# Kernel tuning notes

Measured on AMD Instinct MI355X. Metric: run time of the kernel, lower is better.

Reference implementation:

```python
import jax, jax.numpy as jnp
import numpy as np

IN_F = 1024
OUT_F = 512
BATCH = 256
NO_EDGE_OFFSET_T_NORM = 2.0    # identity element offset for min over [0,1] inputs
NO_EDGE_OFFSET_T_CONORM = -1.0 # identity element offset for max over [0,1] inputs


def setup_inputs() -> dict:
    key = jax.random.key(0)
    k1, k2 = jax.random.split(key)
    # fuzzy truth-value inputs in [0, 1]
    x = jax.random.uniform(k1, (BATCH, IN_F), dtype=jnp.float32)
    # logits for gumbel-softmax edge-type selection (module inits to ones)
    edge_type_count = jnp.ones((OUT_F, IN_F, 2), dtype=jnp.float32)
    # uniform noise used to build gumbel noise deterministically
    uniform_noise = jax.random.uniform(k2, (OUT_F, IN_F, 2), dtype=jnp.float32)
    return {"x": x, "edge_type_count": edge_type_count, "uniform_noise": uniform_noise}


def reference(x, edge_type_count, uniform_noise):
    eps = 1e-10
    # hard gumbel-softmax -> only the argmax index is consumed downstream
    gumbel = -jnp.log(-jnp.log(uniform_noise + eps) + eps)
    idx = jnp.argmax(edge_type_count + gumbel, axis=-1)   # [OUT_F, IN_F]; 0 = edge, 1 = no_edge
    is_no_edge = idx == 1                                  # [OUT_F, IN_F]

    # operators cycle [T_Norm.min, T_Conorm.max] across output nodes
    tnorm = (jnp.arange(OUT_F) % 2) == 0                   # [OUT_F]
    offset = jnp.where(tnorm, NO_EDGE_OFFSET_T_NORM, NO_EDGE_OFFSET_T_CONORM).astype(x.dtype)

    # edge value: x for a real edge, 0 + per-operator no_edge offset otherwise
    vals = jnp.where(is_no_edge[None, :, :], offset[None, :, None], x[:, None, :])  # [B, OUT_F, IN_F]

    # per-node t-norm (min) or t-conorm (max) reduction over in_features
    out = jnp.where(tnorm[None, :], jnp.min(vals, axis=-1), jnp.max(vals, axis=-1))  # [B, OUT_F]
    return out
```

## Files before the change

### kernel.cpp

```cpp
#include <hip/hip_runtime.h>
#include <stdint.h>

#define IN_F   1024
#define OUT_F  512
#define BATCH  256

__global__ __launch_bounds__(256) void mask_kernel(
    const float* __restrict__ etc,
    const float* __restrict__ un,
    unsigned long long* __restrict__ mask_t)
{
    int o = blockIdx.x >> 2;
    int c = blockIdx.x & 3;
    int j = threadIdx.x >> 6;
    int l = threadIdx.x & 63;
    int i = c * 256 + l * 4 + j;
    int p = o * IN_F + i;

    float2 e = ((const float2*)etc)[p];
    float2 u = ((const float2*)un)[p];

    float s0 = u.x + 1e-10f;
    float l0 = (float)log((double)s0);
    float m0 = -l0 + 1e-10f;
    float g0 = -(float)log((double)m0);
    float t0 = e.x + g0;

    float s1 = u.y + 1e-10f;
    float l1 = (float)log((double)s1);
    float m1 = -l1 + 1e-10f;
    float g1 = -(float)log((double)m1);
    float t1 = e.y + g1;

    unsigned long long bits = __ballot(!(t1 > t0));
    if (l == 0) mask_t[o * 16 + c * 4 + j] = bits;
}

__device__ __forceinline__ float csel(unsigned long long m, float xv, float sent) {
    float r;
    asm("v_cndmask_b32 %0, %1, %2, %3" : "=v"(r) : "v"(sent), "v"(xv), "s"(m));
    return r;
}

__global__ __launch_bounds__(256, 8) void reduce_kernel(
    const float* __restrict__ x,
    const unsigned long long* __restrict__ mask_t,
    float* __restrict__ out)
{
    int wave = threadIdx.x >> 6;
    int lane = threadIdx.x & 63;
    int W = blockIdx.x * 4 + wave;
    int b  = __builtin_amdgcn_readfirstlane(W >> 7);
    int r  = W & 127;
    int parity = __builtin_amdgcn_readfirstlane(r & 1);
    int oq = __builtin_amdgcn_readfirstlane(r >> 1);

    const float4* x4 = (const float4*)(x + b * IN_F);

    int o0 = ((oq * 4 + 0) << 1) | parity;
    int o1 = ((oq * 4 + 1) << 1) | parity;
    int o2 = ((oq * 4 + 2) << 1) | parity;
    int o3 = ((oq * 4 + 3) << 1) | parity;
    const unsigned long long* mw0 = mask_t + o0 * 16;
    const unsigned long long* mw1 = mask_t + o1 * 16;
    const unsigned long long* mw2 = mask_t + o2 * 16;
    const unsigned long long* mw3 = mask_t + o3 * 16;

    if (parity == 0) {
        float a0 = 2.0f, a1 = 2.0f, a2 = 2.0f, a3 = 2.0f;
        const float S = 2.0f;
        #pragma unroll
        for (int c = 0; c < 4; ++c) {
            float4 xv = x4[c * 64 + lane];
            a0 = fminf(a0, csel(mw0[c*4+0], xv.x, S));
            a0 = fminf(a0, csel(mw0[c*4+1], xv.y, S));
            a0 = fminf(a0, csel(mw0[c*4+2], xv.z, S));
            a0 = fminf(a0, csel(mw0[c*4+3], xv.w, S));
            a1 = fminf(a1, csel(mw1[c*4+0], xv.x, S));
            a1 = fminf(a1, csel(mw1[c*4+1], xv.y, S));
            a1 = fminf(a1, csel(mw1[c*4+2], xv.z, S));
            a1 = fminf(a1, csel(mw1[c*4+3], xv.w, S));
            a2 = fminf(a2, csel(mw2[c*4+0], xv.x, S));
            a2 = fminf(a2, csel(mw2[c*4+1], xv.y, S));
            a2 = fminf(a2, csel(mw2[c*4+2], xv.z, S));
            a2 = fminf(a2, csel(mw2[c*4+3], xv.w, S));
            a3 = fminf(a3, csel(mw3[c*4+0], xv.x, S));
            a3 = fminf(a3, csel(mw3[c*4+1], xv.y, S));
            a3 = fminf(a3, csel(mw3[c*4+2], xv.z, S));
            a3 = fminf(a3, csel(mw3[c*4+3], xv.w, S));
        }
        #pragma unroll
        for (int d = 32; d; d >>= 1) {
            a0 = fminf(a0, __shfl_xor(a0, d, 64));
            a1 = fminf(a1, __shfl_xor(a1, d, 64));
            a2 = fminf(a2, __shfl_xor(a2, d, 64));
            a3 = fminf(a3, __shfl_xor(a3, d, 64));
        }
        if (lane == 0) {
            float* ob = out + b * OUT_F;
            ob[o0] = a0; ob[o1] = a1; ob[o2] = a2; ob[o3] = a3;
        }
    } else {
        float a0 = -1.0f, a1 = -1.0f, a2 = -1.0f, a3 = -1.0f;
        const float S = -1.0f;
        #pragma unroll
        for (int c = 0; c < 4; ++c) {
            float4 xv = x4[c * 64 + lane];
            a0 = fmaxf(a0, csel(mw0[c*4+0], xv.x, S));
            a0 = fmaxf(a0, csel(mw0[c*4+1], xv.y, S));
            a0 = fmaxf(a0, csel(mw0[c*4+2], xv.z, S));
            a0 = fmaxf(a0, csel(mw0[c*4+3], xv.w, S));
            a1 = fmaxf(a1, csel(mw1[c*4+0], xv.x, S));
            a1 = fmaxf(a1, csel(mw1[c*4+1], xv.y, S));
            a1 = fmaxf(a1, csel(mw1[c*4+2], xv.z, S));
            a1 = fmaxf(a1, csel(mw1[c*4+3], xv.w, S));
            a2 = fmaxf(a2, csel(mw2[c*4+0], xv.x, S));
            a2 = fmaxf(a2, csel(mw2[c*4+1], xv.y, S));
            a2 = fmaxf(a2, csel(mw2[c*4+2], xv.z, S));
            a2 = fmaxf(a2, csel(mw2[c*4+3], xv.w, S));
            a3 = fmaxf(a3, csel(mw3[c*4+0], xv.x, S));
            a3 = fmaxf(a3, csel(mw3[c*4+1], xv.y, S));
            a3 = fmaxf(a3, csel(mw3[c*4+2], xv.z, S));
            a3 = fmaxf(a3, csel(mw3[c*4+3], xv.w, S));
        }
        #pragma unroll
        for (int d = 32; d; d >>= 1) {
            a0 = fmaxf(a0, __shfl_xor(a0, d, 64));
            a1 = fmaxf(a1, __shfl_xor(a1, d, 64));
            a2 = fmaxf(a2, __shfl_xor(a2, d, 64));
            a3 = fmaxf(a3, __shfl_xor(a3, d, 64));
        }
        if (lane == 0) {
            float* ob = out + b * OUT_F;
            ob[o0] = a0; ob[o1] = a1; ob[o2] = a2; ob[o3] = a3;
        }
    }
}

extern "C" void kernel_launch(void* const* d_in, const int* in_sizes, int n_in,
                              void* d_out, int out_size, void* d_ws, size_t ws_size,
                              hipStream_t stream) {
    const float* x   = (const float*)d_in[0];
    const float* etc = (const float*)d_in[1];
    const float* un  = (const float*)d_in[2];
    float* out = (float*)d_out;
    unsigned long long* mask_t = (unsigned long long*)d_ws;

    hipLaunchKernelGGL(mask_kernel, dim3(OUT_F * 4), dim3(256), 0, stream,
                       etc, un, mask_t);
    hipLaunchKernelGGL(reduce_kernel, dim3(BATCH * OUT_F / 4 / 4), dim3(256), 0, stream,
                       x, mask_t, out);
}
```

Before: 79.04 us.

## Process two batch rows per wave, use min3/max3, merge cross-row reductions

```diff
diff --git a/kernel.cpp b/kernel.cpp
--- a/kernel.cpp
+++ b/kernel.cpp
@@ -41,6 +41,16 @@
     asm("v_cndmask_b32 %0, %1, %2, %3" : "=v"(r) : "v"(sent), "v"(xv), "s"(m));
     return r;
 }
+__device__ __forceinline__ float vmin3(float a, float b, float c) {
+    float r;
+    asm("v_min3_f32 %0, %1, %2, %3" : "=v"(r) : "v"(a), "v"(b), "v"(c));
+    return r;
+}
+__device__ __forceinline__ float vmax3(float a, float b, float c) {
+    float r;
+    asm("v_max3_f32 %0, %1, %2, %3" : "=v"(r) : "v"(a), "v"(b), "v"(c));
+    return r;
+}
 
 __global__ __launch_bounds__(256, 8) void reduce_kernel(
     const float* __restrict__ x,
@@ -49,13 +59,14 @@
 {
     int wave = threadIdx.x >> 6;
     int lane = threadIdx.x & 63;
-    int W = blockIdx.x * 4 + wave;
-    int b  = __builtin_amdgcn_readfirstlane(W >> 7);
-    int r  = W & 127;
+    int T = blockIdx.x * 4 + wave;
+    int bp = __builtin_amdgcn_readfirstlane(T >> 7);
+    int r  = T & 127;
     int parity = __builtin_amdgcn_readfirstlane(r & 1);
     int oq = __builtin_amdgcn_readfirstlane(r >> 1);
 
-    const float4* x4 = (const float4*)(x + b * IN_F);
+    const float4* xA = (const float4*)(x + (bp * 2 + 0) * IN_F);
+    const float4* xB = (const float4*)(x + (bp * 2 + 1) * IN_F);
 
     int o0 = ((oq * 4 + 0) << 1) | parity;
     int o1 = ((oq * 4 + 1) << 1) | parity;
@@ -66,73 +77,103 @@
     const unsigned long long* mw2 = mask_t + o2 * 16;
     const unsigned long long* mw3 = mask_t + o3 * 16;
 
+    bool hi = (lane & 32) != 0;
+
     if (parity == 0) {
-        float a0 = 2.0f, a1 = 2.0f, a2 = 2.0f, a3 = 2.0f;
         const float S = 2.0f;
+        float aA0=S, aA1=S, aA2=S, aA3=S;
+        float aB0=S, aB1=S, aB2=S, aB3=S;
         #pragma unroll
         for (int c = 0; c < 4; ++c) {
-            float4 xv = x4[c * 64 + lane];
-            a0 = fminf(a0, csel(mw0[c*4+0], xv.x, S));
-            a0 = fminf(a0, csel(mw0[c*4+1], xv.y, S));
-            a0 = fminf(a0, csel(mw0[c*4+2], xv.z, S));
-            a0 = fminf(a0, csel(mw0[c*4+3], xv.w, S));
-            a1 = fminf(a1, csel(mw1[c*4+0], xv.x, S));
-            a1 = fminf(a1, csel(mw1[c*4+1], xv.y, S));
-            a1 = fminf(a1, csel(mw1[c*4+2], xv.z, S));
-            a1 = fminf(a1, csel(mw1[c*4+3], xv.w, S));
-            a2 = fminf(a2, csel(mw2[c*4+0], xv.x, S));
-            a2 = fminf(a2, csel(mw2[c*4+1], xv.y, S));
-            a2 = fminf(a2, csel(mw2[c*4+2], xv.z, S));
-            a2 = fminf(a2, csel(mw2[c*4+3], xv.w, S));
-            a3 = fminf(a3, csel(mw3[c*4+0], xv.x, S));
-            a3 = fminf(a3, csel(mw3[c*4+1], xv.y, S));
-            a3 = fminf(a3, csel(mw3[c*4+2], xv.z, S));
-            a3 = fminf(a3, csel(mw3[c*4+3], xv.w, S));
+            float4 va = xA[c * 64 + lane];
+            float4 vb = xB[c * 64 + lane];
+            {
+                unsigned long long m0=mw0[c*4+0], m1=mw0[c*4+1], m2=mw0[c*4+2], m3=mw0[c*4+3];
+                aA0 = vmin3(aA0, vmin3(csel(m0,va.x,S), csel(m1,va.y,S), csel(m2,va.z,S)), csel(m3,va.w,S));
+                aB0 = vmin3(aB0, vmin3(csel(m0,vb.x,S), csel(m1,vb.y,S), csel(m2,vb.z,S)), csel(m3,vb.w,S));
+            }
+            {
+                unsigned long long m0=mw1[c*4+0], m1=mw1[c*4+1], m2=mw1[c*4+2], m3=mw1[c*4+3];
+                aA1 = vmin3(aA1, vmin3(csel(m0,va.x,S), csel(m1,va.y,S), csel(m2,va.z,S)), csel(m3,va.w,S));
+                aB1 = vmin3(aB1, vmin3(csel(m0,vb.x,S), csel(m1,vb.y,S), csel(m2,vb.z,S)), csel(m3,vb.w,S));
+            }
+            {
+                unsigned long long m0=mw2[c*4+0], m1=mw2[c*4+1], m2=mw2[c*4+2], m3=mw2[c*4+3];
+                aA2 = vmin3(aA2, vmin3(csel(m0,va.x,S), csel(m1,va.y,S), csel(m2,va.z,S)), csel(m3,va.w,S));
+                aB2 = vmin3(aB2, vmin3(csel(m0,vb.x,S), csel(m1,vb.y,S), csel(m2,vb.z,S)), csel(m3,vb.w,S));
+            }
+            {
+                unsigned long long m0=mw3[c*4+0], m1=mw3[c*4+1], m2=mw3[c*4+2], m3=mw3[c*4+3];
+                aA3 = vmin3(aA3, vmin3(csel(m0,va.x,S), csel(m1,va.y,S), csel(m2,va.z,S)), csel(m3,va.w,S));
+                aB3 = vmin3(aB3, vmin3(csel(m0,vb.x,S), csel(m1,vb.y,S), csel(m2,vb.z,S)), csel(m3,vb.w,S));
+            }
         }
+        float c0 = hi ? aA0 : aB0;  float p0 = __shfl_xor(c0, 32, 64);
+        float c1 = hi ? aA1 : aB1;  float p1 = __shfl_xor(c1, 32, 64);
+        float c2 = hi ? aA2 : aB2;  float p2 = __shfl_xor(c2, 32, 64);
+        float c3 = hi ? aA3 : aB3;  float p3 = __shfl_xor(c3, 32, 64);
+        float z0 = fminf(hi ? aB0 : aA0, p0);
+        float z1 = fminf(hi ? aB1 : aA1, p1);
+        float z2 = fminf(hi ? aB2 : aA2, p2);
+        float z3 = fminf(hi ? aB3 : aA3, p3);
         #pragma unroll
-        for (int d = 32; d; d >>= 1) {
-            a0 = fminf(a0, __shfl_xor(a0, d, 64));
-            a1 = fminf(a1, __shfl_xor(a1, d, 64));
-            a2 = fminf(a2, __shfl_xor(a2, d, 64));
-            a3 = fminf(a3, __shfl_xor(a3, d, 64));
+        for (int d = 16; d; d >>= 1) {
+            z0 = fminf(z0, __shfl_xor(z0, d, 64));
+            z1 = fminf(z1, __shfl_xor(z1, d, 64));
+            z2 = fminf(z2, __shfl_xor(z2, d, 64));
+            z3 = fminf(z3, __shfl_xor(z3, d, 64));
         }
-        if (lane == 0) {
-            float* ob = out + b * OUT_F;
-            ob[o0] = a0; ob[o1] = a1; ob[o2] = a2; ob[o3] = a3;
+        if ((lane & 31) == 0) {
+            float* ob = out + (bp * 2 + (lane >> 5)) * OUT_F;
+            ob[o0] = z0; ob[o1] = z1; ob[o2] = z2; ob[o3] = z3;
         }
     } else {
-        float a0 = -1.0f, a1 = -1.0f, a2 = -1.0f, a3 = -1.0f;
         const float S = -1.0f;
+        float aA0=S, aA1=S, aA2=S, aA3=S;
+        float aB0=S, aB1=S, aB2=S, aB3=S;
         #pragma unroll
         for (int c = 0; c < 4; ++c) {
-            float4 xv = x4[c * 64 + lane];
-            a0 = fmaxf(a0, csel(mw0[c*4+0], xv.x, S));
-            a0 = fmaxf(a0, csel(mw0[c*4+1], xv.y, S));
-            a0 = fmaxf(a0, csel(mw0[c*4+2], xv.z, S));
-            a0 = fmaxf(a0, csel(mw0[c*4+3], xv.w, S));
-            a1 = fmaxf(a1, csel(mw1[c*4+0], xv.x, S));
-            a1 = fmaxf(a1, csel(mw1[c*4+1], xv.y, S));
-            a1 = fmaxf(a1, csel(mw1[c*4+2], xv.z, S));
-            a1 = fmaxf(a1, csel(mw1[c*4+3], xv.w, S));
-            a2 = fmaxf(a2, csel(mw2[c*4+0], xv.x, S));
-            a2 = fmaxf(a2, csel(mw2[c*4+1], xv.y, S));
-            a2 = fmaxf(a2, csel(mw2[c*4+2], xv.z, S));
-            a2 = fmaxf(a2, csel(mw2[c*4+3], xv.w, S));
-            a3 = fmaxf(a3, csel(mw3[c*4+0], xv.x, S));
-            a3 = fmaxf(a3, csel(mw3[c*4+1], xv.y, S));
-            a3 = fmaxf(a3, csel(mw3[c*4+2], xv.z, S));
-            a3 = fmaxf(a3, csel(mw3[c*4+3], xv.w, S));
+            float4 va = xA[c * 64 + lane];
+            float4 vb = xB[c * 64 + lane];
+            {
+                unsigned long long m0=mw0[c*4+0], m1=mw0[c*4+1], m2=mw0[c*4+2], m3=mw0[c*4+3];
+                aA0 = vmax3(aA0, vmax3(csel(m0,va.x,S), csel(m1,va.y,S), csel(m2,va.z,S)), csel(m3,va.w,S));
+                aB0 = vmax3(aB0, vmax3(csel(m0,vb.x,S), csel(m1,vb.y,S), csel(m2,vb.z,S)), csel(m3,vb.w,S));
+            }
+            {
+                unsigned long long m0=mw1[c*4+0], m1=mw1[c*4+1], m2=mw1[c*4+2], m3=mw1[c*4+3];
+                aA1 = vmax3(aA1, vmax3(csel(m0,va.x,S), csel(m1,va.y,S), csel(m2,va.z,S)), csel(m3,va.w,S));
+                aB1 = vmax3(aB1, vmax3(csel(m0,vb.x,S), csel(m1,vb.y,S), csel(m2,vb.z,S)), csel(m3,vb.w,S));
+            }
+            {
+                unsigned long long m0=mw2[c*4+0], m1=mw2[c*4+1], m2=mw2[c*4+2], m3=mw2[c*4+3];
+                aA2 = vmax3(aA2, vmax3(csel(m0,va.x,S), csel(m1,va.y,S), csel(m2,va.z,S)), csel(m3,va.w,S));
+                aB2 = vmax3(aB2, vmax3(csel(m0,vb.x,S), csel(m1,vb.y,S), csel(m2,vb.z,S)), csel(m3,vb.w,S));
+            }
+            {
+                unsigned long long m0=mw3[c*4+0], m1=mw3[c*4+1], m2=mw3[c*4+2], m3=mw3[c*4+3];
+                aA3 = vmax3(aA3, vmax3(csel(m0,va.x,S), csel(m1,va.y,S), csel(m2,va.z,S)), csel(m3,va.w,S));
+                aB3 = vmax3(aB3, vmax3(csel(m0,vb.x,S), csel(m1,vb.y,S), csel(m2,vb.z,S)), csel(m3,vb.w,S));
+            }
         }
+        float c0 = hi ? aA0 : aB0;  float p0 = __shfl_xor(c0, 32, 64);
+        float c1 = hi ? aA1 : aB1;  float p1 = __shfl_xor(c1, 32, 64);
+        float c2 = hi ? aA2 : aB2;  float p2 = __shfl_xor(c2, 32, 64);
+        float c3 = hi ? aA3 : aB3;  float p3 = __shfl_xor(c3, 32, 64);
+        float z0 = fmaxf(hi ? aB0 : aA0, p0);
+        float z1 = fmaxf(hi ? aB1 : aA1, p1);
+        float z2 = fmaxf(hi ? aB2 : aA2, p2);
+        float z3 = fmaxf(hi ? aB3 : aA3, p3);
         #pragma unroll
-        for (int d = 32; d; d >>= 1) {
-            a0 = fmaxf(a0, __shfl_xor(a0, d, 64));
-            a1 = fmaxf(a1, __shfl_xor(a1, d, 64));
-            a2 = fmaxf(a2, __shfl_xor(a2, d, 64));
-            a3 = fmaxf(a3, __shfl_xor(a3, d, 64));
+        for (int d = 16; d; d >>= 1) {
+            z0 = fmaxf(z0, __shfl_xor(z0, d, 64));
+            z1 = fmaxf(z1, __shfl_xor(z1, d, 64));
+            z2 = fmaxf(z2, __shfl_xor(z2, d, 64));
+            z3 = fmaxf(z3, __shfl_xor(z3, d, 64));
         }
-        if (lane == 0) {
-            float* ob = out + b * OUT_F;
-            ob[o0] = a0; ob[o1] = a1; ob[o2] = a2; ob[o3] = a3;
+        if ((lane & 31) == 0) {
+            float* ob = out + (bp * 2 + (lane >> 5)) * OUT_F;
+            ob[o0] = z0; ob[o1] = z1; ob[o2] = z2; ob[o3] = z3;
         }
     }
 }
@@ -148,6 +189,6 @@
 
     hipLaunchKernelGGL(mask_kernel, dim3(OUT_F * 4), dim3(256), 0, stream,
                        etc, un, mask_t);
-    hipLaunchKernelGGL(reduce_kernel, dim3(BATCH * OUT_F / 4 / 4), dim3(256), 0, stream,
+    hipLaunchKernelGGL(reduce_kernel, dim3(BATCH * OUT_F / 8 / 4), dim3(256), 0, stream,
                        x, mask_t, out);
 }
```

New measurement: 77.31 us. 1.02x faster.

## Fuse mask generation and min/max reduction into one kernel with LDS masks

Applied to the files above, without the earlier changes.

```diff
diff --git a/kernel.cpp b/kernel.cpp
--- a/kernel.cpp
+++ b/kernel.cpp
@@ -5,134 +5,149 @@
 #define OUT_F  512
 #define BATCH  256
 
-__global__ __launch_bounds__(256) void mask_kernel(
-    const float* __restrict__ etc,
-    const float* __restrict__ un,
-    unsigned long long* __restrict__ mask_t)
-{
-    int o = blockIdx.x >> 2;
-    int c = blockIdx.x & 3;
-    int j = threadIdx.x >> 6;
-    int l = threadIdx.x & 63;
-    int i = c * 256 + l * 4 + j;
-    int p = o * IN_F + i;
-
-    float2 e = ((const float2*)etc)[p];
-    float2 u = ((const float2*)un)[p];
-
-    float s0 = u.x + 1e-10f;
-    float l0 = (float)log((double)s0);
-    float m0 = -l0 + 1e-10f;
-    float g0 = -(float)log((double)m0);
-    float t0 = e.x + g0;
-
-    float s1 = u.y + 1e-10f;
-    float l1 = (float)log((double)s1);
-    float m1 = -l1 + 1e-10f;
-    float g1 = -(float)log((double)m1);
-    float t1 = e.y + g1;
-
-    unsigned long long bits = __ballot(!(t1 > t0));
-    if (l == 0) mask_t[o * 16 + c * 4 + j] = bits;
-}
-
 __device__ __forceinline__ float csel(unsigned long long m, float xv, float sent) {
     float r;
     asm("v_cndmask_b32 %0, %1, %2, %3" : "=v"(r) : "v"(sent), "v"(xv), "s"(m));
     return r;
 }
+__device__ __forceinline__ float vmin3(float a, float b, float c) {
+    float r;
+    asm("v_min3_f32 %0, %1, %2, %3" : "=v"(r) : "v"(a), "v"(b), "v"(c));
+    return r;
+}
+__device__ __forceinline__ float vmax3(float a, float b, float c) {
+    float r;
+    asm("v_max3_f32 %0, %1, %2, %3" : "=v"(r) : "v"(a), "v"(b), "v"(c));
+    return r;
+}
+__device__ __forceinline__ unsigned long long uniform_u64(unsigned long long m) {
+    unsigned int lo = __builtin_amdgcn_readfirstlane((unsigned int)m);
+    unsigned int hi = __builtin_amdgcn_readfirstlane((unsigned int)(m >> 32));
+    return ((unsigned long long)hi << 32) | lo;
+}
 
-__global__ __launch_bounds__(256, 8) void reduce_kernel(
+__global__ __launch_bounds__(512, 2) void fused_kernel(
     const float* __restrict__ x,
-    const unsigned long long* __restrict__ mask_t,
+    const float* __restrict__ etc,
+    const float* __restrict__ un,
     float* __restrict__ out)
 {
-    int wave = threadIdx.x >> 6;
+    __shared__ unsigned long long lmask[64];
+
+    int oq   = __builtin_amdgcn_readfirstlane(blockIdx.x >> 1);
+    int bh   = __builtin_amdgcn_readfirstlane(blockIdx.x & 1);
+    int wv   = threadIdx.x >> 6;
     int lane = threadIdx.x & 63;
-    int W = blockIdx.x * 4 + wave;
-    int b  = __builtin_amdgcn_readfirstlane(W >> 7);
-    int r  = W & 127;
-    int parity = __builtin_amdgcn_readfirstlane(r & 1);
-    int oq = __builtin_amdgcn_readfirstlane(r >> 1);
 
-    const float4* x4 = (const float4*)(x + b * IN_F);
+    #pragma unroll
+    for (int k = 0; k < 8; ++k) {
+        int W = wv * 8 + k;
+        int s = W >> 4;
+        int c = (W >> 2) & 3;
+        int j = W & 3;
+        int o = oq * 4 + s;
+        int i = c * 256 + lane * 4 + j;
+        int p = o * IN_F + i;
 
-    int o0 = ((oq * 4 + 0) << 1) | parity;
-    int o1 = ((oq * 4 + 1) << 1) | parity;
-    int o2 = ((oq * 4 + 2) << 1) | parity;
-    int o3 = ((oq * 4 + 3) << 1) | parity;
-    const unsigned long long* mw0 = mask_t + o0 * 16;
-    const unsigned long long* mw1 = mask_t + o1 * 16;
-    const unsigned long long* mw2 = mask_t + o2 * 16;
-    const unsigned long long* mw3 = mask_t + o3 * 16;
+        float2 e = ((const float2*)etc)[p];
+        float2 u = ((const float2*)un)[p];
 
-    if (parity == 0) {
-        float a0 = 2.0f, a1 = 2.0f, a2 = 2.0f, a3 = 2.0f;
-        const float S = 2.0f;
+        float s0 = u.x + 1e-10f;
+        float l0 = (float)log((double)s0);
+        float m0 = -l0 + 1e-10f;
+        float g0 = -(float)log((double)m0);
+        float t0 = e.x + g0;
+
+        float s1 = u.y + 1e-10f;
+        float l1 = (float)log((double)s1);
+        float m1 = -l1 + 1e-10f;
+        float g1 = -(float)log((double)m1);
+        float t1 = e.y + g1;
+
+        unsigned long long bits = __ballot(!(t1 > t0));
+        if (lane == 0) lmask[W] = bits;
+    }
+    __syncthreads();
+
+    const float4* xq = (const float4*)x;
+    bool hi = (lane & 32) != 0;
+    int obase = oq * 4;
+
+    for (int tile = 0; tile < 2; ++tile) {
+        int bp0 = (bh << 6) + (wv << 3) + (tile << 2);
+
+        float acc[4][4][2];
+        #pragma unroll
+        for (int q = 0; q < 4; ++q)
+            #pragma unroll
+            for (int s = 0; s < 4; ++s) {
+                float S = (s & 1) ? -1.0f : 2.0f;
+                acc[q][s][0] = S;
+                acc[q][s][1] = S;
+            }
+
         #pragma unroll
         for (int c = 0; c < 4; ++c) {
-            float4 xv = x4[c * 64 + lane];
-            a0 = fminf(a0, csel(mw0[c*4+0], xv.x, S));
-            a0 = fminf(a0, csel(mw0[c*4+1], xv.y, S));
-            a0 = fminf(a0, csel(mw0[c*4+2], xv.z, S));
-            a0 = fminf(a0, csel(mw0[c*4+3], xv.w, S));
-            a1 = fminf(a1, csel(mw1[c*4+0], xv.x, S));
-            a1 = fminf(a1, csel(mw1[c*4+1], xv.y, S));
-            a1 = fminf(a1, csel(mw1[c*4+2], xv.z, S));
-            a1 = fminf(a1, csel(mw1[c*4+3], xv.w, S));
-            a2 = fminf(a2, csel(mw2[c*4+0], xv.x, S));
-            a2 = fminf(a2, csel(mw2[c*4+1], xv.y, S));
-            a2 = fminf(a2, csel(mw2[c*4+2], xv.z, S));
-            a2 = fminf(a2, csel(mw2[c*4+3], xv.w, S));
-            a3 = fminf(a3, csel(mw3[c*4+0], xv.x, S));
-            a3 = fminf(a3, csel(mw3[c*4+1], xv.y, S));
-            a3 = fminf(a3, csel(mw3[c*4+2], xv.z, S));
-            a3 = fminf(a3, csel(mw3[c*4+3], xv.w, S));
+            unsigned long long mk[16];
+            #pragma unroll
+            for (int s = 0; s < 4; ++s)
+                #pragma unroll
+                for (int j = 0; j < 4; ++j)
+                    mk[s * 4 + j] = uniform_u64(lmask[s * 16 + c * 4 + j]);
+
+            #pragma unroll
+            for (int q = 0; q < 4; ++q) {
+                int b0 = (bp0 + q) << 1;
+                float4 va = xq[(b0 + 0) * (IN_F / 4) + c * 64 + lane];
+                float4 vb = xq[(b0 + 1) * (IN_F / 4) + c * 64 + lane];
+                #pragma unroll
+                for (int s = 0; s < 4; ++s) {
+                    float S = (s & 1) ? -1.0f : 2.0f;
+                    float e0a = csel(mk[s*4+0], va.x, S);
+                    float e1a = csel(mk[s*4+1], va.y, S);
+                    float e2a = csel(mk[s*4+2], va.z, S);
+                    float e3a = csel(mk[s*4+3], va.w, S);
+                    float e0b = csel(mk[s*4+0], vb.x, S);
+                    float e1b = csel(mk[s*4+1], vb.y, S);
+                    float e2b = csel(mk[s*4+2], vb.z, S);
+                    float e3b = csel(mk[s*4+3], vb.w, S);
+                    if (s & 1) {
+                        acc[q][s][0] = vmax3(acc[q][s][0], vmax3(e0a, e1a, e2a), e3a);
+                        acc[q][s][1] = vmax3(acc[q][s][1], vmax3(e0b, e1b, e2b), e3b);
+                    } else {
+                        acc[q][s][0] = vmin3(acc[q][s][0], vmin3(e0a, e1a, e2a), e3a);
+                        acc[q][s][1] = vmin3(acc[q][s][1], vmin3(e0b, e1b, e2b), e3b);
+                    }
+                }
+            }
         }
+
         #pragma unroll
-        for (int d = 32; d; d >>= 1) {
-            a0 = fminf(a0, __shfl_xor(a0, d, 64));
-            a1 = fminf(a1, __shfl_xor(a1, d, 64));
-            a2 = fminf(a2, __shfl_xor(a2, d, 64));
-            a3 = fminf(a3, __shfl_xor(a3, d, 64));
-        }
-        if (lane == 0) {
-            float* ob = out + b * OUT_F;
-            ob[o0] = a0; ob[o1] = a1; ob[o2] = a2; ob[o3] = a3;
-        }
-    } else {
-        float a0 = -1.0f, a1 = -1.0f, a2 = -1.0f, a3 = -1.0f;
-        const float S = -1.0f;
-        #pragma unroll
-        for (int c = 0; c < 4; ++c) {
-            float4 xv = x4[c * 64 + lane];
-            a0 = fmaxf(a0, csel(mw0[c*4+0], xv.x, S));
-            a0 = fmaxf(a0, csel(mw0[c*4+1], xv.y, S));
-            a0 = fmaxf(a0, csel(mw0[c*4+2], xv.z, S));
-            a0 = fmaxf(a0, csel(mw0[c*4+3], xv.w, S));
-            a1 = fmaxf(a1, csel(mw1[c*4+0], xv.x, S));
-            a1 = fmaxf(a1, csel(mw1[c*4+1], xv.y, S));
-            a1 = fmaxf(a1, csel(mw1[c*4+2], xv.z, S));
-            a1 = fmaxf(a1, csel(mw1[c*4+3], xv.w, S));
-            a2 = fmaxf(a2, csel(mw2[c*4+0], xv.x, S));
-            a2 = fmaxf(a2, csel(mw2[c*4+1], xv.y, S));
-            a2 = fmaxf(a2, csel(mw2[c*4+2], xv.z, S));
-            a2 = fmaxf(a2, csel(mw2[c*4+3], xv.w, S));
-            a3 = fmaxf(a3, csel(mw3[c*4+0], xv.x, S));
-            a3 = fmaxf(a3, csel(mw3[c*4+1], xv.y, S));
-            a3 = fmaxf(a3, csel(mw3[c*4+2], xv.z, S));
-            a3 = fmaxf(a3, csel(mw3[c*4+3], xv.w, S));
-        }
-        #pragma unroll
-        for (int d = 32; d; d >>= 1) {
-            a0 = fmaxf(a0, __shfl_xor(a0, d, 64));
-            a1 = fmaxf(a1, __shfl_xor(a1, d, 64));
-            a2 = fmaxf(a2, __shfl_xor(a2, d, 64));
-            a3 = fmaxf(a3, __shfl_xor(a3, d, 64));
-        }
-        if (lane == 0) {
-            float* ob = out + b * OUT_F;
-            ob[o0] = a0; ob[o1] = a1; ob[o2] = a2; ob[o3] = a3;
+        for (int q = 0; q < 4; ++q) {
+            int b0 = (bp0 + q) << 1;
+            float z[4];
+            #pragma unroll
+            for (int s = 0; s < 4; ++s) {
+                float aA = acc[q][s][0], aB = acc[q][s][1];
+                float cr = hi ? aA : aB;
+                float pp = __shfl_xor(cr, 32, 64);
+                float zz = hi ? aB : aA;
+                if (s & 1) {
+                    zz = fmaxf(zz, pp);
+                    #pragma unroll
+                    for (int d = 16; d; d >>= 1) zz = fmaxf(zz, __shfl_xor(zz, d, 64));
+                } else {
+                    zz = fminf(zz, pp);
+                    #pragma unroll
+                    for (int d = 16; d; d >>= 1) zz = fminf(zz, __shfl_xor(zz, d, 64));
+                }
+                z[s] = zz;
+            }
+            if ((lane & 31) == 0) {
+                int b = b0 + (lane >> 5);
+                float4 o4 = make_float4(z[0], z[1], z[2], z[3]);
+                *((float4*)(out + b * OUT_F + obase)) = o4;
+            }
         }
     }
 }
@@ -144,10 +159,8 @@
     const float* etc = (const float*)d_in[1];
     const float* un  = (const float*)d_in[2];
     float* out = (float*)d_out;
-    unsigned long long* mask_t = (unsigned long long*)d_ws;
+    (void)d_ws; (void)ws_size;
 
-    hipLaunchKernelGGL(mask_kernel, dim3(OUT_F * 4), dim3(256), 0, stream,
-                       etc, un, mask_t);
-    hipLaunchKernelGGL(reduce_kernel, dim3(BATCH * OUT_F / 4 / 4), dim3(256), 0, stream,
-                       x, mask_t, out);
+    hipLaunchKernelGGL(fused_kernel, dim3(256), dim3(512), 0, stream,
+                       x, etc, un, out);
 }
```

Result: slower. 87.21 us (+10.3%).
